# Kernel optimization log

Measured on AMD Instinct MI355X. Metric: run time of the kernel, lower is better.

Reference implementation:

```python
import jax, jax.numpy as jnp
import numpy as np

N_QUBITS = 8
NUM_HEADS = 2
EPS = 1e-5
TWO_PI = 6.283185307179586


def _rx(state, wire, theta, n):
    # state: (B, 2**n) complex64; theta: (B,) float. PennyLane wire 0 = MSB.
    B = state.shape[0]
    st = state.reshape(B, 2 ** wire, 2, 2 ** (n - 1 - wire))
    c = jnp.cos(theta * 0.5).astype(state.dtype)[:, None, None]
    s = ((-1j) * jnp.sin(theta * 0.5).astype(state.dtype))[:, None, None]
    a0 = st[:, :, 0, :]
    a1 = st[:, :, 1, :]
    return jnp.stack([c * a0 + s * a1, s * a0 + c * a1], axis=2).reshape(B, -1)


def _cnot(state, ctrl, tgt, n):
    B = state.shape[0]
    st = state.reshape((B,) + (2,) * n)
    ax_c = ctrl + 1
    ax_t = tgt + 1
    s0 = jnp.take(st, 0, axis=ax_c)
    s1 = jnp.take(st, 1, axis=ax_c)
    ft = ax_t - 1 if ax_t > ax_c else ax_t
    s1 = jnp.flip(s1, axis=ft)
    return jnp.stack([s0, s1], axis=ax_c).reshape(B, -1)


def _vqc(x, weights):
    # AngleEmbedding (RX) + BasicEntanglerLayers (RX per wire + CNOT ring) -> <Z_i>.
    # x: (B, n) angles; weights: (L, n). Returns (B, n) real expvals.
    B, n = x.shape
    state = jnp.zeros((B, 2 ** n), dtype=jnp.complex64).at[:, 0].set(1.0)
    for w in range(n):
        state = _rx(state, w, x[:, w], n)
    pairs = [(i, (i + 1) % n) for i in range(n)] if n > 2 else ([(0, 1)] if n == 2 else [])
    for l in range(weights.shape[0]):
        for w in range(n):
            state = _rx(state, w, jnp.broadcast_to(weights[l, w], (B,)), n)
        for cw, tw in pairs:
            state = _cnot(state, cw, tw, n)
    probs = (state.real ** 2 + state.imag ** 2).reshape((B,) + (2,) * n)
    zs = []
    for w in range(n):
        axes = tuple(a for a in range(1, n + 1) if a != w + 1)
        p = jnp.sum(probs, axis=axes)  # (B, 2)
        zs.append(p[:, 0] - p[:, 1])
    return jnp.stack(zs, axis=-1)


def _layernorm(x, g, b):
    m = jnp.mean(x, axis=-1, keepdims=True)
    v = jnp.mean((x - m) ** 2, axis=-1, keepdims=True)
    return (x - m) / jnp.sqrt(v + EPS) * g + b


def setup_inputs() -> dict:
    key = jax.random.key(0)
    ks = jax.random.split(key, 10)
    E = N_QUBITS
    x = jax.random.normal(ks[0], (64, 256, E), dtype=jnp.float32)
    # TorchLayer default init: uniform(0, 2*pi)
    Wq = jax.random.uniform(ks[1], (1, E), dtype=jnp.float32) * TWO_PI
    Wk = jax.random.uniform(ks[2], (1, E), dtype=jnp.float32) * TWO_PI
    Wv = jax.random.uniform(ks[3], (1, E), dtype=jnp.float32) * TWO_PI
    Wc = jax.random.uniform(ks[4], (1, E), dtype=jnp.float32) * TWO_PI
    Wf = jax.random.uniform(ks[5], (1, E), dtype=jnp.float32) * TWO_PI
    w1 = jax.random.normal(ks[6], (E, E), dtype=jnp.float32) * 0.3
    b1 = jax.random.normal(ks[7], (E,), dtype=jnp.float32) * 0.05
    w2 = jax.random.normal(ks[8], (E, E), dtype=jnp.float32) * 0.3
    b2 = jax.random.normal(ks[9], (E,), dtype=jnp.float32) * 0.05
    gamma1 = jnp.ones((E,), dtype=jnp.float32)
    beta1 = jnp.zeros((E,), dtype=jnp.float32)
    gamma2 = jnp.ones((E,), dtype=jnp.float32)
    beta2 = jnp.zeros((E,), dtype=jnp.float32)
    return {"x": x, "Wq": Wq, "Wk": Wk, "Wv": Wv, "Wc": Wc, "Wf": Wf,
            "w1": w1, "b1": b1, "w2": w2, "b2": b2,
            "gamma1": gamma1, "beta1": beta1, "gamma2": gamma2, "beta2": beta2}


def reference(x, Wq, Wk, Wv, Wc, Wf, w1, b1, w2, b2, gamma1, beta1, gamma2, beta2):
    B, S, E = x.shape
    H = NUM_HEADS
    dk = E // H
    tok = x.reshape(B * S, E)
    Q = _vqc(tok, Wq).reshape(B, S, E)
    K = _vqc(tok, Wk).reshape(B, S, E)
    V = _vqc(tok, Wv).reshape(B, S, E)
    split = lambda t: t.reshape(B, S, H, dk).transpose(0, 2, 1, 3)
    scores = jnp.einsum('bhqd,bhkd->bhqk', split(Q), split(K)) / jnp.sqrt(jnp.float32(dk))
    attn = jax.nn.softmax(scores, axis=-1)  # dropout = identity in eval
    ctx = jnp.einsum('bhqk,bhkd->bhqd', attn, split(V)).transpose(0, 2, 1, 3).reshape(B, S, E)
    attn_out = _vqc(ctx.reshape(B * S, E), Wc).reshape(B, S, E)
    x = _layernorm(x + attn_out, gamma1, beta1)
    h = x @ w1.T + b1                       # linear1 (no activation in FeedForwardQuantum)
    hq = _vqc(h.reshape(B * S, -1), Wf).reshape(B, S, -1)
    ff = hq @ w2.T + b2                     # linear2
    x = _layernorm(x + ff, gamma2, beta2)
    return x
```

## Files before the change

### kernel.cpp

```cpp
#include <hip/hip_runtime.h>


#define SEQ 256
#define EMB 8
#define QG  64
#define NSPLIT 4

static __device__ __forceinline__ void load8f(const float* __restrict__ p, float v[8]) {
    float4 a = *reinterpret_cast<const float4*>(p);
    float4 b = *reinterpret_cast<const float4*>(p + 4);
    v[0] = a.x; v[1] = a.y; v[2] = a.z; v[3] = a.w;
    v[4] = b.x; v[5] = b.y; v[6] = b.z; v[7] = b.w;
}

static __device__ __forceinline__ void store8f(float* __restrict__ p, const float v[8]) {
    *reinterpret_cast<float4*>(p)     = make_float4(v[0], v[1], v[2], v[3]);
    *reinterpret_cast<float4*>(p + 4) = make_float4(v[4], v[5], v[6], v[7]);
}

static __device__ __forceinline__ void vqc8(const float in[8], const float W[8], float z[8]) {
    float c[8];
#pragma unroll
    for (int i = 0; i < 8; ++i) c[i] = __cosf(in[i] + W[i]);
    float t = c[1];
#pragma unroll
    for (int i = 2; i < 8; ++i) t *= c[i];
    z[0] = t;
    float acc = c[0];
#pragma unroll
    for (int i = 1; i < 8; ++i) { acc *= c[i]; z[i] = acc; }
}

static __device__ __forceinline__ void ln8(const float r[8], const float g[8], const float be[8], float o[8]) {
    float m = 0.f;
#pragma unroll
    for (int i = 0; i < 8; ++i) m += r[i];
    m *= 0.125f;
    float var = 0.f;
#pragma unroll
    for (int i = 0; i < 8; ++i) { float d = r[i] - m; var += d * d; }
    var *= 0.125f;
    float inv = rsqrtf(var + 1e-5f);
#pragma unroll
    for (int i = 0; i < 8; ++i) o[i] = (r[i] - m) * inv * g[i] + be[i];
}

__global__ __launch_bounds__(512) void vitq_kernel(
    const float* __restrict__ x,
    const float* __restrict__ Wq, const float* __restrict__ Wk,
    const float* __restrict__ Wv, const float* __restrict__ Wc,
    const float* __restrict__ Wf,
    const float* __restrict__ w1, const float* __restrict__ b1,
    const float* __restrict__ w2, const float* __restrict__ b2,
    const float* __restrict__ g1, const float* __restrict__ be1,
    const float* __restrict__ g2, const float* __restrict__ be2,
    float* __restrict__ out)
{
    __shared__ float Ks[SEQ][EMB];
    __shared__ float Vs[SEQ][EMB];
    __shared__ float P[NSPLIT][2 * QG][5];

    const int bi  = blockIdx.x;
    const int b   = bi >> 2;
    const int g   = bi & 3;
    const int tid = threadIdx.x;
    const int p   = tid & 127;
    const int j   = tid >> 7;
    const int sl  = p & 63;
    const int h   = p >> 6;
    const int s   = g * QG + sl;

    const float* xb = x + ((size_t)b * SEQ) * EMB;

    float xq[8], wrow[8], q[8];
    load8f(xb + (size_t)s * EMB, xq);
    load8f(Wq, wrow);
    vqc8(xq, wrow, q);

    {
        const int t = tid & 255;
        float xs[8], kv[8];
        load8f(xb + (size_t)t * EMB, xs);
        if (tid < 256) {
            load8f(Wk, wrow);
            vqc8(xs, wrow, kv);
            store8f(&Ks[t][0], kv);
        } else {
            load8f(Wv, wrow);
            vqc8(xs, wrow, kv);
            store8f(&Vs[t][0], kv);
        }
    }
    __syncthreads();

    const int ho = 4 * h;
    float qh[4];
#pragma unroll
    for (int d = 0; d < 4; ++d) qh[d] = q[ho + d] * 0.5f;

    float l = 0.f, acc0 = 0.f, acc1 = 0.f, acc2 = 0.f, acc3 = 0.f;
    const int k0 = j * 64;
#pragma unroll 8
    for (int kk = k0; kk < k0 + 64; ++kk) {
        float4 kr = *reinterpret_cast<const float4*>(&Ks[kk][ho]);
        float4 vr = *reinterpret_cast<const float4*>(&Vs[kk][ho]);
        float sc = qh[0] * kr.x + qh[1] * kr.y + qh[2] * kr.z + qh[3] * kr.w;
        float e  = __expf(sc);
        l    += e;
        acc0 += e * vr.x;
        acc1 += e * vr.y;
        acc2 += e * vr.z;
        acc3 += e * vr.w;
    }
    P[j][p][0] = l;
    P[j][p][1] = acc0;
    P[j][p][2] = acc1;
    P[j][p][3] = acc2;
    P[j][p][4] = acc3;
    __syncthreads();

    if (tid < QG) {
        float ctx[8];
#pragma unroll
        for (int hh = 0; hh < 2; ++hh) {
            const int pp = hh * QG + tid;
            float ll = 0.f, a0 = 0.f, a1 = 0.f, a2 = 0.f, a3 = 0.f;
#pragma unroll
            for (int jj = 0; jj < NSPLIT; ++jj) {
                ll += P[jj][pp][0];
                a0 += P[jj][pp][1];
                a1 += P[jj][pp][2];
                a2 += P[jj][pp][3];
                a3 += P[jj][pp][4];
            }
            float inv = 1.f / ll;
            ctx[4 * hh + 0] = a0 * inv;
            ctx[4 * hh + 1] = a1 * inv;
            ctx[4 * hh + 2] = a2 * inv;
            ctx[4 * hh + 3] = a3 * inv;
        }

        float ao[8];
        load8f(Wc, wrow);
        vqc8(ctx, wrow, ao);

        float r[8];
#pragma unroll
        for (int i = 0; i < 8; ++i) r[i] = xq[i] + ao[i];

        float gg[8], be[8], x1[8];
        load8f(g1, gg); load8f(be1, be);
        ln8(r, gg, be, x1);

        float wf[64], bias[8];
#pragma unroll
        for (int i = 0; i < 64; ++i) wf[i] = w1[i];
        load8f(b1, bias);
        float hv[8];
#pragma unroll
        for (int jj = 0; jj < 8; ++jj) {
            float a = bias[jj];
#pragma unroll
            for (int i = 0; i < 8; ++i) a += x1[i] * wf[jj * 8 + i];
            hv[jj] = a;
        }

        float hq[8];
        load8f(Wf, wrow);
        vqc8(hv, wrow, hq);

#pragma unroll
        for (int i = 0; i < 64; ++i) wf[i] = w2[i];
        load8f(b2, bias);
        float r2[8];
#pragma unroll
        for (int jj = 0; jj < 8; ++jj) {
            float a = bias[jj];
#pragma unroll
            for (int i = 0; i < 8; ++i) a += hq[i] * wf[jj * 8 + i];
            r2[jj] = x1[jj] + a;
        }

        float o[8];
        load8f(g2, gg); load8f(be2, be);
        ln8(r2, gg, be, o);

        store8f(out + ((size_t)(b * SEQ + s)) * EMB, o);
    }
}

extern "C" void kernel_launch(void* const* d_in, const int* in_sizes, int n_in,
                              void* d_out, int out_size, void* d_ws, size_t ws_size,
                              hipStream_t stream) {
    const float* x   = (const float*)d_in[0];
    const float* Wq  = (const float*)d_in[1];
    const float* Wk  = (const float*)d_in[2];
    const float* Wv  = (const float*)d_in[3];
    const float* Wc  = (const float*)d_in[4];
    const float* Wf  = (const float*)d_in[5];
    const float* w1  = (const float*)d_in[6];
    const float* b1  = (const float*)d_in[7];
    const float* w2  = (const float*)d_in[8];
    const float* b2  = (const float*)d_in[9];
    const float* g1  = (const float*)d_in[10];
    const float* be1 = (const float*)d_in[11];
    const float* g2  = (const float*)d_in[12];
    const float* be2 = (const float*)d_in[13];
    float* out = (float*)d_out;

    const int B = in_sizes[0] / (SEQ * EMB);
    vitq_kernel<<<B * 4, 512, 0, stream>>>(x, Wq, Wk, Wv, Wc, Wf, w1, b1, w2, b2,
                                           g1, be1, g2, be2, out);
}
```

Baseline: 85.53 us.

## Double key-split threads to 1024 and parallelize softmax partial reduction

Block size doubles to 1024 threads, and each thread handles 32 keys instead of 64 in the attention loop. The softmax uses exp2 with a log2e-folded scale. The partial-sum merge is spread over 128 threads through a new shared context buffer, with an extra barrier. The epilogue reloads x for its token and streams the linear weights row by row instead of holding 64 registers. The aim is more latency hiding per block and a shorter serial tail, at the cost of extra sync and lower occupancy per CU, since each block now runs 1024 threads.

```diff
diff --git a/kernel.cpp b/kernel.cpp
--- a/kernel.cpp
+++ b/kernel.cpp
@@ -4,7 +4,7 @@
 #define SEQ 256
 #define EMB 8
 #define QG  64
-#define NSPLIT 4
+#define NSPLIT 8
 
 static __device__ __forceinline__ void load8f(const float* __restrict__ p, float v[8]) {
     float4 a = *reinterpret_cast<const float4*>(p);
@@ -45,7 +45,7 @@
     for (int i = 0; i < 8; ++i) o[i] = (r[i] - m) * inv * g[i] + be[i];
 }
 
-__global__ __launch_bounds__(512) void vitq_kernel(
+__global__ __launch_bounds__(1024) void vitq_kernel(
     const float* __restrict__ x,
     const float* __restrict__ Wq, const float* __restrict__ Wk,
     const float* __restrict__ Wv, const float* __restrict__ Wc,
@@ -59,6 +59,7 @@
     __shared__ float Ks[SEQ][EMB];
     __shared__ float Vs[SEQ][EMB];
     __shared__ float P[NSPLIT][2 * QG][5];
+    __shared__ float Cs[QG][EMB];
 
     const int bi  = blockIdx.x;
     const int b   = bi >> 2;
@@ -77,7 +78,7 @@
     load8f(Wq, wrow);
     vqc8(xq, wrow, q);
 
-    {
+    if (tid < 512) {
         const int t = tid & 255;
         float xs[8], kv[8];
         load8f(xb + (size_t)t * EMB, xs);
@@ -96,16 +97,16 @@
     const int ho = 4 * h;
     float qh[4];
 #pragma unroll
-    for (int d = 0; d < 4; ++d) qh[d] = q[ho + d] * 0.5f;
+    for (int d = 0; d < 4; ++d) qh[d] = q[ho + d] * (0.5f * 1.44269504f);
 
     float l = 0.f, acc0 = 0.f, acc1 = 0.f, acc2 = 0.f, acc3 = 0.f;
-    const int k0 = j * 64;
+    const int k0 = j * 32;
 #pragma unroll 8
-    for (int kk = k0; kk < k0 + 64; ++kk) {
+    for (int kk = k0; kk < k0 + 32; ++kk) {
         float4 kr = *reinterpret_cast<const float4*>(&Ks[kk][ho]);
         float4 vr = *reinterpret_cast<const float4*>(&Vs[kk][ho]);
         float sc = qh[0] * kr.x + qh[1] * kr.y + qh[2] * kr.z + qh[3] * kr.w;
-        float e  = __expf(sc);
+        float e  = __builtin_amdgcn_exp2f(sc);
         l    += e;
         acc0 += e * vr.x;
         acc1 += e * vr.y;
@@ -119,49 +120,55 @@
     P[j][p][4] = acc3;
     __syncthreads();
 
+    if (tid < 128) {
+        float ll = 0.f, a0 = 0.f, a1 = 0.f, a2 = 0.f, a3 = 0.f;
+#pragma unroll
+        for (int jj = 0; jj < NSPLIT; ++jj) {
+            ll += P[jj][tid][0];
+            a0 += P[jj][tid][1];
+            a1 += P[jj][tid][2];
+            a2 += P[jj][tid][3];
+            a3 += P[jj][tid][4];
+        }
+        const int sl2 = tid & 63;
+        const int ho2 = 4 * (tid >> 6);
+        float inv = 1.f / ll;
+        Cs[sl2][ho2 + 0] = a0 * inv;
+        Cs[sl2][ho2 + 1] = a1 * inv;
+        Cs[sl2][ho2 + 2] = a2 * inv;
+        Cs[sl2][ho2 + 3] = a3 * inv;
+    }
+    __syncthreads();
+
     if (tid < QG) {
         float ctx[8];
-#pragma unroll
-        for (int hh = 0; hh < 2; ++hh) {
-            const int pp = hh * QG + tid;
-            float ll = 0.f, a0 = 0.f, a1 = 0.f, a2 = 0.f, a3 = 0.f;
-#pragma unroll
-            for (int jj = 0; jj < NSPLIT; ++jj) {
-                ll += P[jj][pp][0];
-                a0 += P[jj][pp][1];
-                a1 += P[jj][pp][2];
-                a2 += P[jj][pp][3];
-                a3 += P[jj][pp][4];
-            }
-            float inv = 1.f / ll;
-            ctx[4 * hh + 0] = a0 * inv;
-            ctx[4 * hh + 1] = a1 * inv;
-            ctx[4 * hh + 2] = a2 * inv;
-            ctx[4 * hh + 3] = a3 * inv;
-        }
+        load8f(&Cs[tid][0], ctx);
 
         float ao[8];
         load8f(Wc, wrow);
         vqc8(ctx, wrow, ao);
 
+        float xr[8];
+        load8f(xb + (size_t)(g * QG + tid) * EMB, xr);
+
         float r[8];
 #pragma unroll
-        for (int i = 0; i < 8; ++i) r[i] = xq[i] + ao[i];
+        for (int i = 0; i < 8; ++i) r[i] = xr[i] + ao[i];
 
         float gg[8], be[8], x1[8];
         load8f(g1, gg); load8f(be1, be);
         ln8(r, gg, be, x1);
 
-        float wf[64], bias[8];
-#pragma unroll
-        for (int i = 0; i < 64; ++i) wf[i] = w1[i];
+        float bias[8];
         load8f(b1, bias);
         float hv[8];
 #pragma unroll
         for (int jj = 0; jj < 8; ++jj) {
+            float wr[8];
+            load8f(w1 + jj * 8, wr);
             float a = bias[jj];
 #pragma unroll
-            for (int i = 0; i < 8; ++i) a += x1[i] * wf[jj * 8 + i];
+            for (int i = 0; i < 8; ++i) a += x1[i] * wr[i];
             hv[jj] = a;
         }
 
@@ -169,15 +176,15 @@
         load8f(Wf, wrow);
         vqc8(hv, wrow, hq);
 
-#pragma unroll
-        for (int i = 0; i < 64; ++i) wf[i] = w2[i];
         load8f(b2, bias);
         float r2[8];
 #pragma unroll
         for (int jj = 0; jj < 8; ++jj) {
+            float wr[8];
+            load8f(w2 + jj * 8, wr);
             float a = bias[jj];
 #pragma unroll
-            for (int i = 0; i < 8; ++i) a += hq[i] * wf[jj * 8 + i];
+            for (int i = 0; i < 8; ++i) a += hq[i] * wr[i];
             r2[jj] = x1[jj] + a;
         }
 
@@ -185,7 +192,7 @@
         load8f(g2, gg); load8f(be2, be);
         ln8(r2, gg, be, o);
 
-        store8f(out + ((size_t)(b * SEQ + s)) * EMB, o);
+        store8f(out + ((size_t)(b * SEQ + g * QG + tid)) * EMB, o);
     }
 }
 
@@ -209,6 +216,6 @@
     float* out = (float*)d_out;
 
     const int B = in_sizes[0] / (SEQ * EMB);
-    vitq_kernel<<<B * 4, 512, 0, stream>>>(x, Wq, Wk, Wv, Wc, Wf, w1, b1, w2, b2,
-                                           g1, be1, g2, be2, out);
-}
+    vitq_kernel<<<B * 4, 1024, 0, stream>>>(x, Wq, Wk, Wv, Wc, Wf, w1, b1, w2, b2,
+                                            g1, be1, g2, be2, out);
+}
```

New measurement: 86.09 us. No clear change (+0.6%).
